# Kernel tuning notes

Hardware: AMD Instinct MI355X
Metric: run time of the kernel (lower is better)

The kernel has to match this reference:

```python
import jax, jax.numpy as jnp
import numpy as np

HD = 64        # hidden_dim
H = 4          # heads
N = 50000      # nodes
E = 400000     # edges (before self loops)
NEG_ATT = 0.2  # GATConv attention LeakyReLU slope (PyG default)
NEG_ACT = 0.01 # nn.LeakyReLU() default slope
EPS = 1e-5     # BatchNorm eps


def _bn(x, gamma, beta):
    # training-mode BatchNorm1d over node dimension (biased variance)
    mu = x.mean(0)
    var = x.var(0)
    return gamma * (x - mu) * jax.lax.rsqrt(var + EPS) + beta


def _gatconv(h_in, src, dst, W, a_src, a_dst, bias, heads, outc, concat):
    n = h_in.shape[0]
    h = (h_in @ W.T).reshape(n, heads, outc)              # [N,H,C]
    al_s = jnp.einsum('nhc,hc->nh', h, a_src)             # [N,H]
    al_d = jnp.einsum('nhc,hc->nh', h, a_dst)
    e = jax.nn.leaky_relu(al_s[src] + al_d[dst], NEG_ATT) # [E',H]
    # softmax over incoming edges of each destination node
    m = jax.lax.stop_gradient(jax.ops.segment_max(e, dst, num_segments=n))
    ex = jnp.exp(e - m[dst])
    den = jax.ops.segment_sum(ex, dst, num_segments=n)
    alpha = ex / den[dst]                                  # [E',H]
    out = jax.ops.segment_sum(h[src] * alpha[..., None], dst, num_segments=n)
    out = out.reshape(n, heads * outc) if concat else out.mean(axis=1)
    return out + bias


def setup_inputs() -> dict:
    ks = jax.random.split(jax.random.key(0), 20)
    s = 0.1
    d = {
        'x': jax.random.normal(ks[0], (N, 2 * HD), jnp.float32),
        'edge_index': jax.random.randint(ks[1], (2, E), 0, N, jnp.int64),
        'W1': jax.random.normal(ks[2], (H * HD, 2 * HD), jnp.float32) * s,
        'a1s': jax.random.normal(ks[3], (H, HD), jnp.float32) * s,
        'a1d': jax.random.normal(ks[4], (H, HD), jnp.float32) * s,
        'b1': jnp.zeros((H * HD,), jnp.float32),
        'W2': jax.random.normal(ks[5], (H * HD, H * HD), jnp.float32) * s,
        'a2s': jax.random.normal(ks[6], (H, HD), jnp.float32) * s,
        'a2d': jax.random.normal(ks[7], (H, HD), jnp.float32) * s,
        'b2': jnp.zeros((H * HD,), jnp.float32),
        'W3': jax.random.normal(ks[8], (1 * HD, H * HD), jnp.float32) * s,
        'a3s': jax.random.normal(ks[9], (1, HD), jnp.float32) * s,
        'a3d': jax.random.normal(ks[10], (1, HD), jnp.float32) * s,
        'b3': jnp.zeros((HD,), jnp.float32),
        'gamma': jnp.ones((H * HD,), jnp.float32),
        'beta': jnp.zeros((H * HD,), jnp.float32),
    }
    return d


def reference(x, edge_index, W1, a1s, a1d, b1, W2, a2s, a2d, b2,
              W3, a3s, a3d, b3, gamma, beta):
    n = x.shape[0]
    loop = jnp.arange(n, dtype=edge_index.dtype)
    src = jnp.concatenate([edge_index[0], loop])  # add_self_loops=True
    dst = jnp.concatenate([edge_index[1], loop])

    h = _gatconv(x, src, dst, W1, a1s, a1d, b1, H, HD, True)
    h = jax.nn.leaky_relu(_bn(h, gamma, beta), NEG_ACT)

    # single middle residual block (num_layers=3); dropout is identity (eval)
    res = h
    h = _gatconv(h, src, dst, W2, a2s, a2d, b2, H, HD, True)
    h = jax.nn.leaky_relu(_bn(h, gamma, beta), NEG_ACT)
    h = h + res

    out = _gatconv(h, src, dst, W3, a3s, a3d, b3, 1, HD, False)
    return out
```

## Files before the change

### kernel.cpp

```cpp
#include <hip/hip_runtime.h>
#include <hip/hip_bf16.h>

#define NEG_ATT 0.2f
#define NEG_ACT 0.01f

typedef __attribute__((ext_vector_type(8))) short short8;
typedef __attribute__((ext_vector_type(4))) float f32x4;

__device__ __forceinline__ unsigned short f2bf(float f) {
    unsigned int u = __float_as_uint(f);
    unsigned int r = (u + 0x7fff + ((u >> 16) & 1)) >> 16;
    return (unsigned short)r;
}
__device__ __forceinline__ float b2f(unsigned short h) {
    return __uint_as_float((unsigned int)h << 16);
}


#define SCAN_CHUNK 1024
__global__ void scan1(const int* __restrict__ deg, int* __restrict__ offs,
                      int* blocksum, int Nn) {
    __shared__ int sh[256];
    int b = blockIdx.x, t = threadIdx.x;
    int base = b * SCAN_CHUNK + t * 4;
    int v[4];
    int s = 0;
    for (int j = 0; j < 4; j++) {
        int idx = base + j;
        v[j] = (idx < Nn) ? deg[idx] + 1 : 0;
        s += v[j];
    }
    sh[t] = s;
    __syncthreads();
    for (int off = 1; off < 256; off <<= 1) {
        int x = (t >= off) ? sh[t - off] : 0;
        __syncthreads();
        sh[t] += x;
        __syncthreads();
    }
    int excl = sh[t] - s;
    if (t == 255) blocksum[b] = sh[255];
    int run = excl;
    for (int j = 0; j < 4; j++) {
        int idx = base + j;
        if (idx < Nn) offs[idx] = run;
        run += v[j];
    }
}

__global__ void scan23(int* __restrict__ offs, const int* __restrict__ bsum,
                       int* __restrict__ cursor, int Nn, int G) {
    int i = blockIdx.x * 256 + threadIdx.x;
    if (i > Nn) return;
    int g = i >> 10;
    int basev = 0;
    for (int k = 0; k < g; k++) basev += bsum[k];
    if (i == Nn) {
        int tot = basev;
        for (int k = g; k < G; k++) tot += bsum[k];
        offs[Nn] = tot;
        return;
    }
    int v = offs[i] + basev;
    offs[i] = v;
    cursor[i] = v;
}

__global__ void fill_csr(const int* __restrict__ ei, int* cursor, int* csr, int E, int Nn) {
    int t = blockIdx.x * 256 + threadIdx.x;
    if (t < E) {
        int s = ei[t];
        int d = ei[E + t];
        int p = atomicAdd(&cursor[d], 1);
        csr[p] = s;
    } else if (t < E + Nn) {
        int nn = t - E;
        int p = atomicAdd(&cursor[nn], 1);
        csr[p] = nn;
    }
}


__global__ __launch_bounds__(256) void prep_all(
    int* __restrict__ deg, const int* __restrict__ ei, int E,
    const float* __restrict__ x, unsigned short* __restrict__ xb, int nx, int nxpad,
    const float* __restrict__ w1, unsigned short* __restrict__ o1, int n1,
    const float* __restrict__ w2, unsigned short* __restrict__ o2, int n2,
    const float* __restrict__ w3, unsigned short* __restrict__ o3, int n3) {
    int id = blockIdx.x * 256 + threadIdx.x;
    int nconv = (nxpad + n1 + n2 + n3) / 8;
    if (id >= nconv) {
        int e = id - nconv;
        if (e < E) atomicAdd(&deg[ei[E + e]], 1);
        return;
    }
    int i = id * 8;
    const float* in;
    unsigned short* out;
    if (i < nxpad) {
        if (i >= nx) {
            *(ushort4*)&xb[i] = make_ushort4(0, 0, 0, 0);
            *(ushort4*)&xb[i + 4] = make_ushort4(0, 0, 0, 0);
            return;
        }
        in = x + i; out = xb + i;
    } else {
        int j = i - nxpad;
        if (j < n1) { in = w1 + j; out = o1 + j; }
        else if (j < n1 + n2) { in = w2 + (j - n1); out = o2 + (j - n1); }
        else { in = w3 + (j - n1 - n2); out = o3 + (j - n1 - n2); }
    }
    float4 a = *(const float4*)in;
    float4 b = *(const float4*)(in + 4);
    *(ushort4*)out = make_ushort4(f2bf(a.x), f2bf(a.y), f2bf(a.z), f2bf(a.w));
    *(ushort4*)(out + 4) = make_ushort4(f2bf(b.x), f2bf(b.y), f2bf(b.z), f2bf(b.w));
}

template <bool RES>
__device__ __forceinline__ unsigned bnpack2(unsigned short ya, unsigned short yb_,
                                            float sca, float scb, float sha, float shb,
                                            unsigned short ra, unsigned short rb_) {
    float v0 = sca * b2f(ya) + sha; v0 = v0 > 0.f ? v0 : NEG_ACT * v0;
    float v1 = scb * b2f(yb_) + shb; v1 = v1 > 0.f ? v1 : NEG_ACT * v1;
    if (RES) { v0 += b2f(ra); v1 += b2f(rb_); }
    return ((unsigned)f2bf(v1) << 16) | f2bf(v0);
}


template <int K, int CO, int HEADS, bool FUSE, bool FRES, bool FWOUT>
__global__ __launch_bounds__(256) void gemm_mfma(
    const unsigned short* __restrict__ Xb, const unsigned short* __restrict__ Wb,
    unsigned short* __restrict__ Hb, const float* __restrict__ a_s,
    const float* __restrict__ a_d, float* __restrict__ als, float* __restrict__ ald,
    const unsigned short* __restrict__ Yb_in, unsigned short* __restrict__ RWbuf,
    const float* __restrict__ scale, const float* __restrict__ shift, int Nn) {
    constexpr int BM = 128, BK = 64, LD = 72, SLD = 68;
    __shared__ __align__(16) char smem[4 * 32 * SLD * 4];
    unsigned short* As = (unsigned short*)smem;
    unsigned short* Bs = As + BM * LD;
    int tid = threadIdx.x;
    int wave = tid >> 6, lane = tid & 63;
    int quad = lane >> 4, l16 = lane & 15;
    int mt, hd;
    if (HEADS == 4) {
        int gm = gridDim.x >> 2;
        int gm8 = gm & ~7;
        int nfull = gm8 * 4;
        int id = blockIdx.x;
        if (id < nfull) {
            int r = id & 31;
            mt = (id >> 5) * 8 + (r & 7);
            hd = r >> 3;
        } else {
            int t2 = id - nfull;
            mt = gm8 + (t2 >> 2);
            hd = t2 & 3;
        }
    } else {
        mt = blockIdx.x;
        hd = 0;
    }
    int m0 = mt * BM, n0 = hd * 64;
    int arow = tid >> 3;
    int achk = (tid & 7) * 8;
    f32x4 acc[2][4] = {};
    for (int k0 = 0; k0 < K; k0 += BK) {
        __syncthreads();
        if (FUSE) {
            int cb = k0 + achk;
            float4 sc0 = *(const float4*)&scale[cb];
            float4 sc1 = *(const float4*)&scale[cb + 4];
            float4 sh0 = *(const float4*)&shift[cb];
            float4 sh1 = *(const float4*)&shift[cb + 4];
#pragma unroll
            for (int p = 0; p < 4; p++) {
                int r = arow + p * 32;
                int m = m0 + r;
                uint4 o = make_uint4(0, 0, 0, 0);
                if (m < Nn) {
                    ushort4 ua = *(const ushort4*)&Yb_in[(size_t)m * 256 + cb];
                    ushort4 ub = *(const ushort4*)&Yb_in[(size_t)m * 256 + cb + 4];
                    ushort4 ra = make_ushort4(0, 0, 0, 0), rb = ra;
                    if (FRES) {
                        ra = *(const ushort4*)&RWbuf[(size_t)m * 256 + cb];
                        rb = *(const ushort4*)&RWbuf[(size_t)m * 256 + cb + 4];
                    }
                    o.x = bnpack2<FRES>(ua.x, ua.y, sc0.x, sc0.y, sh0.x, sh0.y, ra.x, ra.y);
                    o.y = bnpack2<FRES>(ua.z, ua.w, sc0.z, sc0.w, sh0.z, sh0.w, ra.z, ra.w);
                    o.z = bnpack2<FRES>(ub.x, ub.y, sc1.x, sc1.y, sh1.x, sh1.y, rb.x, rb.y);
                    o.w = bnpack2<FRES>(ub.z, ub.w, sc1.z, sc1.w, sh1.z, sh1.w, rb.z, rb.w);
                    if (FWOUT && hd == 0)
                        *(uint4*)&RWbuf[(size_t)m * 256 + cb] = o;
                }
                *(uint4*)&As[r * LD + achk] = o;
            }
        } else {
#pragma unroll
            for (int p = 0; p < 4; p++) {
                int r = arow + p * 32;
                *(int4*)&As[r * LD + achk] = *(const int4*)&Xb[(size_t)(m0 + r) * K + k0 + achk];
            }
        }
#pragma unroll
        for (int p = 0; p < 2; p++) {
            int r = arow + p * 32;
            *(int4*)&Bs[r * LD + achk] = *(const int4*)&Wb[(size_t)(n0 + r) * K + k0 + achk];
        }
        __syncthreads();
#pragma unroll
        for (int ks = 0; ks < 2; ks++) {
            short8 af[2], bfr[4];
#pragma unroll
            for (int i = 0; i < 2; i++)
                af[i] = *(const short8*)&As[(wave * 32 + i * 16 + l16) * LD + ks * 32 + quad * 8];
#pragma unroll
            for (int j = 0; j < 4; j++)
                bfr[j] = *(const short8*)&Bs[(j * 16 + l16) * LD + ks * 32 + quad * 8];
#pragma unroll
            for (int i = 0; i < 2; i++)
#pragma unroll
                for (int j = 0; j < 4; j++)
                    acc[i][j] = __builtin_amdgcn_mfma_f32_16x16x32_bf16(af[i], bfr[j], acc[i][j], 0, 0, 0);
        }
    }
    __syncthreads();

    float asv[4], adv[4];
#pragma unroll
    for (int j = 0; j < 4; j++) {
        asv[j] = a_s[hd * 64 + j * 16 + l16];
        adv[j] = a_d[hd * 64 + j * 16 + l16];
    }
#pragma unroll
    for (int i = 0; i < 2; i++)
#pragma unroll
        for (int r = 0; r < 4; r++) {
            float ps = acc[i][0][r] * asv[0] + acc[i][1][r] * asv[1] +
                       acc[i][2][r] * asv[2] + acc[i][3][r] * asv[3];
            float pd = acc[i][0][r] * adv[0] + acc[i][1][r] * adv[1] +
                       acc[i][2][r] * adv[2] + acc[i][3][r] * adv[3];
#pragma unroll
            for (int mm = 1; mm < 16; mm <<= 1) {
                ps += __shfl_xor(ps, mm);
                pd += __shfl_xor(pd, mm);
            }
            if (l16 == 0) {
                int m = m0 + wave * 32 + i * 16 + quad * 4 + r;
                als[m * HEADS + hd] = ps;
                ald[m * HEADS + hd] = pd;
            }
        }

    float* stg = (float*)smem + wave * 32 * SLD;
#pragma unroll
    for (int i = 0; i < 2; i++)
#pragma unroll
        for (int j = 0; j < 4; j++)
#pragma unroll
            for (int r = 0; r < 4; r++)
                stg[(i * 16 + quad * 4 + r) * SLD + j * 16 + l16] = acc[i][j][r];
    int g = lane >> 3, c8 = (lane & 7) * 8;
#pragma unroll
    for (int p = 0; p < 4; p++) {
        int row = p * 8 + g;
        float4 v0 = *(const float4*)&stg[row * SLD + c8];
        float4 v1 = *(const float4*)&stg[row * SLD + c8 + 4];
        uint4 o;
        o.x = ((unsigned)f2bf(v0.y) << 16) | f2bf(v0.x);
        o.y = ((unsigned)f2bf(v0.w) << 16) | f2bf(v0.z);
        o.z = ((unsigned)f2bf(v1.y) << 16) | f2bf(v1.x);
        o.w = ((unsigned)f2bf(v1.w) << 16) | f2bf(v1.z);
        *(uint4*)&Hb[(size_t)(m0 + wave * 32 + row) * CO + n0 + c8] = o;
    }
}


#define EDGE4(sA, sB, sC, sD)                                                        \
    {                                                                                \
        float a0 = als[(sA)*4 + hd], a1 = als[(sB)*4 + hd];                          \
        float a2 = als[(sC)*4 + hd], a3 = als[(sD)*4 + hd];                          \
        ushort4 h0 = *(const ushort4*)&Hb[(size_t)(sA)*256 + c4];                    \
        ushort4 h1 = *(const ushort4*)&Hb[(size_t)(sB)*256 + c4];                    \
        ushort4 h2 = *(const ushort4*)&Hb[(size_t)(sC)*256 + c4];                    \
        ushort4 h3 = *(const ushort4*)&Hb[(size_t)(sD)*256 + c4];                    \
        float e0 = a0 + aldn; e0 = e0 > 0.f ? e0 : NEG_ATT * e0;                     \
        float e1 = a1 + aldn; e1 = e1 > 0.f ? e1 : NEG_ATT * e1;                     \
        float e2 = a2 + aldn; e2 = e2 > 0.f ? e2 : NEG_ATT * e2;                     \
        float e3 = a3 + aldn; e3 = e3 > 0.f ? e3 : NEG_ATT * e3;                     \
        float w0 = __expf(e0), w1 = __expf(e1), w2 = __expf(e2), w3 = __expf(e3);    \
        den += (w0 + w1) + (w2 + w3);                                                \
        acc.x += w0 * b2f(h0.x) + w1 * b2f(h1.x) + w2 * b2f(h2.x) + w3 * b2f(h3.x);  \
        acc.y += w0 * b2f(h0.y) + w1 * b2f(h1.y) + w2 * b2f(h2.y) + w3 * b2f(h3.y);  \
        acc.z += w0 * b2f(h0.z) + w1 * b2f(h1.z) + w2 * b2f(h2.z) + w3 * b2f(h3.z);  \
        acc.w += w0 * b2f(h0.w) + w1 * b2f(h1.w) + w2 * b2f(h2.w) + w3 * b2f(h3.w);  \
    }

__global__ __launch_bounds__(256) void aggregate_h4(
    const unsigned short* __restrict__ Hb, const float* __restrict__ als,
    const float* __restrict__ ald, const int* __restrict__ offs,
    const int* __restrict__ csr, unsigned short* __restrict__ Yb, int Nn) {
    int wave = threadIdx.x >> 6;
    int lane = threadIdx.x & 63;
    int n = blockIdx.x * 4 + wave;
    if (n >= Nn) return;
    int hd = lane >> 4;
    int c4 = lane * 4;
    float aldn = ald[n * 4 + hd];
    int beg = offs[n], end = offs[n + 1];
    float4 acc = make_float4(0.f, 0.f, 0.f, 0.f);
    float den = 0.f;
    for (int b = beg; b < end; b += 64) {
        int cnt = min(64, end - b);
        int idx = 0;
        if (lane < cnt) idx = csr[b + lane];
        int j = 0;
        for (; j + 8 <= cnt; j += 8) {
            int s0 = __shfl(idx, j), s1 = __shfl(idx, j + 1);
            int s2 = __shfl(idx, j + 2), s3 = __shfl(idx, j + 3);
            int s4 = __shfl(idx, j + 4), s5 = __shfl(idx, j + 5);
            int s6 = __shfl(idx, j + 6), s7 = __shfl(idx, j + 7);
            EDGE4(s0, s1, s2, s3);
            EDGE4(s4, s5, s6, s7);
        }
        for (; j + 4 <= cnt; j += 4) {
            int s0 = __shfl(idx, j), s1 = __shfl(idx, j + 1);
            int s2 = __shfl(idx, j + 2), s3 = __shfl(idx, j + 3);
            EDGE4(s0, s1, s2, s3);
        }
        for (; j < cnt; j++) {
            int s = __shfl(idx, j);
            float e = als[s * 4 + hd] + aldn;
            e = e > 0.f ? e : NEG_ATT * e;
            float w = __expf(e);
            den += w;
            ushort4 hv = *(const ushort4*)&Hb[(size_t)s * 256 + c4];
            acc.x += w * b2f(hv.x); acc.y += w * b2f(hv.y);
            acc.z += w * b2f(hv.z); acc.w += w * b2f(hv.w);
        }
    }
    float inv = 1.f / den;
    *(ushort4*)&Yb[(size_t)n * 256 + c4] = make_ushort4(
        f2bf(acc.x * inv), f2bf(acc.y * inv), f2bf(acc.z * inv), f2bf(acc.w * inv));
}

__global__ __launch_bounds__(256) void aggregate_h1(
    const unsigned short* __restrict__ Hb, const float* __restrict__ als,
    const float* __restrict__ ald, const int* __restrict__ offs,
    const int* __restrict__ csr, const float* __restrict__ bias,
    float* __restrict__ Yout, int Nn) {
    int wave = threadIdx.x >> 6;
    int lane = threadIdx.x & 63;
    int sub = lane >> 4, lane16 = lane & 15;
    int n = blockIdx.x * 16 + wave * 4 + sub;
    if (n >= Nn) return;
    int c4 = lane16 * 4;
    float aldn = ald[n];
    int beg = offs[n], end = offs[n + 1];
    float4 acc = make_float4(0.f, 0.f, 0.f, 0.f);
    float den = 0.f;
    for (int b = beg; b < end; b += 16) {
        int cnt = min(16, end - b);
        int idx = 0;
        if (lane16 < cnt) idx = csr[b + lane16];
        int j = 0;
        for (; j + 4 <= cnt; j += 4) {
            int s0 = __shfl(idx, (sub << 4) + j);
            int s1 = __shfl(idx, (sub << 4) + j + 1);
            int s2 = __shfl(idx, (sub << 4) + j + 2);
            int s3 = __shfl(idx, (sub << 4) + j + 3);
            float a0 = als[s0], a1 = als[s1], a2 = als[s2], a3 = als[s3];
            ushort4 h0 = *(const ushort4*)&Hb[(size_t)s0 * 64 + c4];
            ushort4 h1 = *(const ushort4*)&Hb[(size_t)s1 * 64 + c4];
            ushort4 h2 = *(const ushort4*)&Hb[(size_t)s2 * 64 + c4];
            ushort4 h3 = *(const ushort4*)&Hb[(size_t)s3 * 64 + c4];
            float e0 = a0 + aldn; e0 = e0 > 0.f ? e0 : NEG_ATT * e0;
            float e1 = a1 + aldn; e1 = e1 > 0.f ? e1 : NEG_ATT * e1;
            float e2 = a2 + aldn; e2 = e2 > 0.f ? e2 : NEG_ATT * e2;
            float e3 = a3 + aldn; e3 = e3 > 0.f ? e3 : NEG_ATT * e3;
            float w0 = __expf(e0), w1 = __expf(e1), w2 = __expf(e2), w3 = __expf(e3);
            den += (w0 + w1) + (w2 + w3);
            acc.x += w0 * b2f(h0.x) + w1 * b2f(h1.x) + w2 * b2f(h2.x) + w3 * b2f(h3.x);
            acc.y += w0 * b2f(h0.y) + w1 * b2f(h1.y) + w2 * b2f(h2.y) + w3 * b2f(h3.y);
            acc.z += w0 * b2f(h0.z) + w1 * b2f(h1.z) + w2 * b2f(h2.z) + w3 * b2f(h3.z);
            acc.w += w0 * b2f(h0.w) + w1 * b2f(h1.w) + w2 * b2f(h2.w) + w3 * b2f(h3.w);
        }
        for (; j < cnt; j++) {
            int s = __shfl(idx, (sub << 4) + j);
            float e = als[s] + aldn;
            e = e > 0.f ? e : NEG_ATT * e;
            float w = __expf(e);
            den += w;
            ushort4 hv = *(const ushort4*)&Hb[(size_t)s * 64 + c4];
            acc.x += w * b2f(hv.x); acc.y += w * b2f(hv.y);
            acc.z += w * b2f(hv.z); acc.w += w * b2f(hv.w);
        }
    }
    float inv = 1.f / den;
    float4 bv = *(const float4*)&bias[c4];
    float4 o = make_float4(acc.x * inv + bv.x, acc.y * inv + bv.y,
                           acc.z * inv + bv.z, acc.w * inv + bv.w);
    *(float4*)&Yout[(size_t)n * 64 + c4] = o;
}


__global__ __launch_bounds__(256) void bn_stats(const unsigned short* __restrict__ Yb,
                                                float* __restrict__ partial, int Nn) {
    __shared__ float red[4 * 512];
    int t = threadIdx.x;
    int g = blockIdx.x;
    int rows_per = (Nn + gridDim.x - 1) / gridDim.x;
    int r0 = g * rows_per;
    int r1 = min(r0 + rows_per, Nn);
    int sub = t >> 6;
    int c4 = (t & 63) * 4;
    float4 s = make_float4(0.f, 0.f, 0.f, 0.f);
    float4 q = make_float4(0.f, 0.f, 0.f, 0.f);
    for (int r = r0 + sub; r < r1; r += 4) {
        ushort4 u = *(const ushort4*)&Yb[(size_t)r * 256 + c4];
        float vx = b2f(u.x), vy = b2f(u.y), vz = b2f(u.z), vw = b2f(u.w);
        s.x += vx; s.y += vy; s.z += vz; s.w += vw;
        q.x += vx * vx; q.y += vy * vy; q.z += vz * vz; q.w += vw * vw;
    }
    float* rs = &red[sub * 512];
    rs[c4 + 0] = s.x; rs[c4 + 1] = s.y; rs[c4 + 2] = s.z; rs[c4 + 3] = s.w;
    rs[256 + c4 + 0] = q.x; rs[256 + c4 + 1] = q.y;
    rs[256 + c4 + 2] = q.z; rs[256 + c4 + 3] = q.w;
    __syncthreads();
    float v0 = red[t] + red[512 + t] + red[1024 + t] + red[1536 + t];
    float v1 = red[256 + t] + red[768 + t] + red[1280 + t] + red[1792 + t];
    partial[(size_t)g * 512 + t] = v0;
    partial[(size_t)g * 512 + 256 + t] = v1;
}

__global__ __launch_bounds__(256) void bn_reduce_final(
    const float* __restrict__ partial, int NP, const float* __restrict__ gamma,
    const float* __restrict__ beta, float* scale, float* shift, int Nn) {
    __shared__ float sh[8];
    int ch = blockIdx.x;
    int t = threadIdx.x;
    int wave = t >> 6, lane = t & 63;
    float s = 0.f, q = 0.f;
    for (int i = t; i < NP; i += 256) {
        s += partial[(size_t)i * 512 + ch];
        q += partial[(size_t)i * 512 + 256 + ch];
    }
    for (int off = 32; off; off >>= 1) {
        s += __shfl_down(s, off);
        q += __shfl_down(q, off);
    }
    if (lane == 0) { sh[wave] = s; sh[4 + wave] = q; }
    __syncthreads();
    if (t == 0) {
        s = sh[0] + sh[1] + sh[2] + sh[3];
        q = sh[4] + sh[5] + sh[6] + sh[7];
        float inv_n = 1.f / (float)Nn;
        float mu = s * inv_n;
        float var = q * inv_n - mu * mu;
        float sc = gamma[ch] * rsqrtf(var + 1e-5f);
        scale[ch] = sc;
        shift[ch] = beta[ch] - mu * sc;
    }
}


extern "C" void kernel_launch(void* const* d_in, const int* in_sizes, int n_in,
                              void* d_out, int out_size, void* d_ws, size_t ws_size,
                              hipStream_t stream) {
    const float* x    = (const float*)d_in[0];
    const int*   ei   = (const int*)d_in[1];
    const float* W1   = (const float*)d_in[2];
    const float* a1s  = (const float*)d_in[3];
    const float* a1d  = (const float*)d_in[4];
    const float* W2   = (const float*)d_in[6];
    const float* a2s  = (const float*)d_in[7];
    const float* a2d  = (const float*)d_in[8];
    const float* W3   = (const float*)d_in[10];
    const float* a3s  = (const float*)d_in[11];
    const float* a3d  = (const float*)d_in[12];
    const float* b3   = (const float*)d_in[13];
    const float* gamma = (const float*)d_in[14];
    const float* beta  = (const float*)d_in[15];
    float* out = (float*)d_out;

    const int Nn = in_sizes[0] / 128;
    const int E  = in_sizes[1] / 2;
    const int Ep = E + Nn;
    const int Mpad = (Nn + 127) & ~127;

    size_t off = 0;
    char* base = (char*)d_ws;
    auto alloc = [&](size_t bytes) -> void* {
        void* p = base + off;
        off = (off + bytes + 255) & ~(size_t)255;
        return p;
    };
    unsigned short* Hb   = (unsigned short*)alloc((size_t)Mpad * 256 * 2);
    unsigned short* Yb   = (unsigned short*)alloc((size_t)Nn * 256 * 2);
    unsigned short* xb1  = (unsigned short*)alloc((size_t)Mpad * 128 * 2);
    unsigned short* xbig = (unsigned short*)alloc((size_t)Mpad * 256 * 2);
    unsigned short* wb1  = (unsigned short*)alloc((size_t)256 * 128 * 2);
    unsigned short* wb2  = (unsigned short*)alloc((size_t)256 * 256 * 2);
    unsigned short* wb3  = (unsigned short*)alloc((size_t)64 * 256 * 2);
    float* als    = (float*)alloc((size_t)Mpad * 4 * 4);
    float* ald    = (float*)alloc((size_t)Mpad * 4 * 4);
    int*   deg    = (int*)alloc((size_t)Nn * 4);
    int*   offs   = (int*)alloc((size_t)(Nn + 1) * 4);
    int*   cursor = (int*)alloc((size_t)Nn * 4);
    int*   bsum   = (int*)alloc(64 * 4);
    int*   csr    = (int*)alloc((size_t)Ep * 4);
    const int NP = 1024;
    float* partial = (float*)alloc((size_t)NP * 512 * 4);
    float* scale  = (float*)alloc(256 * 4);
    float* shift  = (float*)alloc(256 * 4);
    (void)ws_size;

    const int G = (Nn + SCAN_CHUNK - 1) / SCAN_CHUNK;

    hipMemsetAsync(deg, 0, (size_t)Nn * 4, stream);
    {
        int nxpad = Mpad * 128;
        int wtot = 256 * 128 + 256 * 256 + 64 * 256;
        int nconv = (nxpad + wtot) / 8;
        prep_all<<<(nconv + E + 255) / 256, 256, 0, stream>>>(
            deg, ei, E, x, xb1, Nn * 128, nxpad,
            W1, wb1, 256 * 128, W2, wb2, 256 * 256, W3, wb3, 64 * 256);
    }

    scan1<<<G, 256, 0, stream>>>(deg, offs, bsum, Nn);
    scan23<<<(Nn + 1 + 255) / 256, 256, 0, stream>>>(offs, bsum, cursor, Nn, G);
    fill_csr<<<(Ep + 255) / 256, 256, 0, stream>>>(ei, cursor, csr, E, Nn);

    const int gm = Mpad / 128;
    const int nagg4 = (Nn + 3) / 4;
    const int nagg1 = (Nn + 15) / 16;

    gemm_mfma<128, 256, 4, false, false, false><<<gm * 4, 256, 0, stream>>>(
        xb1, wb1, Hb, a1s, a1d, als, ald, nullptr, nullptr, nullptr, nullptr, 0);
    aggregate_h4<<<nagg4, 256, 0, stream>>>(Hb, als, ald, offs, csr, Yb, Nn);
    bn_stats<<<NP, 256, 0, stream>>>(Yb, partial, Nn);
    bn_reduce_final<<<256, 256, 0, stream>>>(partial, NP, gamma, beta, scale, shift, Nn);

    gemm_mfma<256, 256, 4, true, false, true><<<gm * 4, 256, 0, stream>>>(
        nullptr, wb2, Hb, a2s, a2d, als, ald, Yb, xbig, scale, shift, Nn);
    aggregate_h4<<<nagg4, 256, 0, stream>>>(Hb, als, ald, offs, csr, Yb, Nn);
    bn_stats<<<NP, 256, 0, stream>>>(Yb, partial, Nn);
    bn_reduce_final<<<256, 256, 0, stream>>>(partial, NP, gamma, beta, scale, shift, Nn);

    gemm_mfma<256, 64, 1, true, true, false><<<gm, 256, 0, stream>>>(
        nullptr, wb3, Hb, a3s, a3d, als, ald, Yb, xbig, scale, shift, Nn);
    aggregate_h1<<<nagg1, 256, 0, stream>>>(Hb, als, ald, offs, csr, b3, out, Nn);
}
```

Baseline: 329.1 us.

## Fuse BatchNorm statistics into aggregation and use hardware bf16 pack conversion

```diff
diff --git a/kernel.cpp b/kernel.cpp
--- a/kernel.cpp
+++ b/kernel.cpp
@@ -7,13 +7,13 @@
 typedef __attribute__((ext_vector_type(8))) short short8;
 typedef __attribute__((ext_vector_type(4))) float f32x4;
 
-__device__ __forceinline__ unsigned short f2bf(float f) {
-    unsigned int u = __float_as_uint(f);
-    unsigned int r = (u + 0x7fff + ((u >> 16) & 1)) >> 16;
-    return (unsigned short)r;
-}
 __device__ __forceinline__ float b2f(unsigned short h) {
     return __uint_as_float((unsigned int)h << 16);
+}
+__device__ __forceinline__ unsigned cvt_pk_bf16(float lo, float hi) {
+    unsigned r;
+    asm("v_cvt_pk_bf16_f32 %0, %1, %2" : "=v"(r) : "v"(lo), "v"(hi));
+    return r;
 }
 
 
@@ -112,8 +112,12 @@
     }
     float4 a = *(const float4*)in;
     float4 b = *(const float4*)(in + 4);
-    *(ushort4*)out = make_ushort4(f2bf(a.x), f2bf(a.y), f2bf(a.z), f2bf(a.w));
-    *(ushort4*)(out + 4) = make_ushort4(f2bf(b.x), f2bf(b.y), f2bf(b.z), f2bf(b.w));
+    uint4 o;
+    o.x = cvt_pk_bf16(a.x, a.y);
+    o.y = cvt_pk_bf16(a.z, a.w);
+    o.z = cvt_pk_bf16(b.x, b.y);
+    o.w = cvt_pk_bf16(b.z, b.w);
+    *(uint4*)out = o;
 }
 
 template <bool RES>
@@ -123,7 +127,7 @@
     float v0 = sca * b2f(ya) + sha; v0 = v0 > 0.f ? v0 : NEG_ACT * v0;
     float v1 = scb * b2f(yb_) + shb; v1 = v1 > 0.f ? v1 : NEG_ACT * v1;
     if (RES) { v0 += b2f(ra); v1 += b2f(rb_); }
-    return ((unsigned)f2bf(v1) << 16) | f2bf(v0);
+    return cvt_pk_bf16(v0, v1);
 }
 
 
@@ -266,10 +270,10 @@
         float4 v0 = *(const float4*)&stg[row * SLD + c8];
         float4 v1 = *(const float4*)&stg[row * SLD + c8 + 4];
         uint4 o;
-        o.x = ((unsigned)f2bf(v0.y) << 16) | f2bf(v0.x);
-        o.y = ((unsigned)f2bf(v0.w) << 16) | f2bf(v0.z);
-        o.z = ((unsigned)f2bf(v1.y) << 16) | f2bf(v1.x);
-        o.w = ((unsigned)f2bf(v1.w) << 16) | f2bf(v1.z);
+        o.x = cvt_pk_bf16(v0.x, v0.y);
+        o.y = cvt_pk_bf16(v0.z, v0.w);
+        o.z = cvt_pk_bf16(v1.x, v1.y);
+        o.w = cvt_pk_bf16(v1.z, v1.w);
         *(uint4*)&Hb[(size_t)(m0 + wave * 32 + row) * CO + n0 + c8] = o;
     }
 }
@@ -298,49 +302,68 @@
 __global__ __launch_bounds__(256) void aggregate_h4(
     const unsigned short* __restrict__ Hb, const float* __restrict__ als,
     const float* __restrict__ ald, const int* __restrict__ offs,
-    const int* __restrict__ csr, unsigned short* __restrict__ Yb, int Nn) {
+    const int* __restrict__ csr, unsigned short* __restrict__ Yb,
+    float* __restrict__ S, int Nn) {
+    __shared__ float red[4 * 512];
     int wave = threadIdx.x >> 6;
     int lane = threadIdx.x & 63;
-    int n = blockIdx.x * 4 + wave;
-    if (n >= Nn) return;
     int hd = lane >> 4;
     int c4 = lane * 4;
-    float aldn = ald[n * 4 + hd];
-    int beg = offs[n], end = offs[n + 1];
-    float4 acc = make_float4(0.f, 0.f, 0.f, 0.f);
-    float den = 0.f;
-    for (int b = beg; b < end; b += 64) {
-        int cnt = min(64, end - b);
-        int idx = 0;
-        if (lane < cnt) idx = csr[b + lane];
-        int j = 0;
-        for (; j + 8 <= cnt; j += 8) {
-            int s0 = __shfl(idx, j), s1 = __shfl(idx, j + 1);
-            int s2 = __shfl(idx, j + 2), s3 = __shfl(idx, j + 3);
-            int s4 = __shfl(idx, j + 4), s5 = __shfl(idx, j + 5);
-            int s6 = __shfl(idx, j + 6), s7 = __shfl(idx, j + 7);
-            EDGE4(s0, s1, s2, s3);
-            EDGE4(s4, s5, s6, s7);
-        }
-        for (; j + 4 <= cnt; j += 4) {
-            int s0 = __shfl(idx, j), s1 = __shfl(idx, j + 1);
-            int s2 = __shfl(idx, j + 2), s3 = __shfl(idx, j + 3);
-            EDGE4(s0, s1, s2, s3);
-        }
-        for (; j < cnt; j++) {
-            int s = __shfl(idx, j);
-            float e = als[s * 4 + hd] + aldn;
-            e = e > 0.f ? e : NEG_ATT * e;
-            float w = __expf(e);
-            den += w;
-            ushort4 hv = *(const ushort4*)&Hb[(size_t)s * 256 + c4];
-            acc.x += w * b2f(hv.x); acc.y += w * b2f(hv.y);
-            acc.z += w * b2f(hv.z); acc.w += w * b2f(hv.w);
-        }
-    }
-    float inv = 1.f / den;
-    *(ushort4*)&Yb[(size_t)n * 256 + c4] = make_ushort4(
-        f2bf(acc.x * inv), f2bf(acc.y * inv), f2bf(acc.z * inv), f2bf(acc.w * inv));
+    float4 bs = make_float4(0.f, 0.f, 0.f, 0.f);
+    float4 bq = make_float4(0.f, 0.f, 0.f, 0.f);
+    for (int n = blockIdx.x * 4 + wave; n < Nn; n += gridDim.x * 4) {
+        float aldn = ald[n * 4 + hd];
+        int beg = offs[n], end = offs[n + 1];
+        float4 acc = make_float4(0.f, 0.f, 0.f, 0.f);
+        float den = 0.f;
+        for (int b = beg; b < end; b += 64) {
+            int cnt = min(64, end - b);
+            int idx = 0;
+            if (lane < cnt) idx = csr[b + lane];
+            int j = 0;
+            for (; j + 8 <= cnt; j += 8) {
+                int s0 = __shfl(idx, j), s1 = __shfl(idx, j + 1);
+                int s2 = __shfl(idx, j + 2), s3 = __shfl(idx, j + 3);
+                int s4 = __shfl(idx, j + 4), s5 = __shfl(idx, j + 5);
+                int s6 = __shfl(idx, j + 6), s7 = __shfl(idx, j + 7);
+                EDGE4(s0, s1, s2, s3);
+                EDGE4(s4, s5, s6, s7);
+            }
+            for (; j + 4 <= cnt; j += 4) {
+                int s0 = __shfl(idx, j), s1 = __shfl(idx, j + 1);
+                int s2 = __shfl(idx, j + 2), s3 = __shfl(idx, j + 3);
+                EDGE4(s0, s1, s2, s3);
+            }
+            for (; j < cnt; j++) {
+                int s = __shfl(idx, j);
+                float e = als[s * 4 + hd] + aldn;
+                e = e > 0.f ? e : NEG_ATT * e;
+                float w = __expf(e);
+                den += w;
+                ushort4 hv = *(const ushort4*)&Hb[(size_t)s * 256 + c4];
+                acc.x += w * b2f(hv.x); acc.y += w * b2f(hv.y);
+                acc.z += w * b2f(hv.z); acc.w += w * b2f(hv.w);
+            }
+        }
+        float inv = 1.f / den;
+        float yx = acc.x * inv, yy = acc.y * inv, yz = acc.z * inv, yw = acc.w * inv;
+        uint2 o;
+        o.x = cvt_pk_bf16(yx, yy);
+        o.y = cvt_pk_bf16(yz, yw);
+        *(uint2*)&Yb[(size_t)n * 256 + c4] = o;
+        bs.x += yx; bs.y += yy; bs.z += yz; bs.w += yw;
+        bq.x += yx * yx; bq.y += yy * yy; bq.z += yz * yz; bq.w += yw * yw;
+    }
+    float* rs = &red[wave * 512];
+    rs[c4 + 0] = bs.x; rs[c4 + 1] = bs.y; rs[c4 + 2] = bs.z; rs[c4 + 3] = bs.w;
+    rs[256 + c4 + 0] = bq.x; rs[256 + c4 + 1] = bq.y;
+    rs[256 + c4 + 2] = bq.z; rs[256 + c4 + 3] = bq.w;
+    __syncthreads();
+    int t = threadIdx.x;
+    float v0 = red[t] + red[512 + t] + red[1024 + t] + red[1536 + t];
+    float v1 = red[256 + t] + red[768 + t] + red[1280 + t] + red[1792 + t];
+    atomicAdd(&S[t], v0);
+    atomicAdd(&S[256 + t], v1);
 }
 
 __global__ __launch_bounds__(256) void aggregate_h1(
@@ -403,63 +426,16 @@
 }
 
 
-__global__ __launch_bounds__(256) void bn_stats(const unsigned short* __restrict__ Yb,
-                                                float* __restrict__ partial, int Nn) {
-    __shared__ float red[4 * 512];
-    int t = threadIdx.x;
-    int g = blockIdx.x;
-    int rows_per = (Nn + gridDim.x - 1) / gridDim.x;
-    int r0 = g * rows_per;
-    int r1 = min(r0 + rows_per, Nn);
-    int sub = t >> 6;
-    int c4 = (t & 63) * 4;
-    float4 s = make_float4(0.f, 0.f, 0.f, 0.f);
-    float4 q = make_float4(0.f, 0.f, 0.f, 0.f);
-    for (int r = r0 + sub; r < r1; r += 4) {
-        ushort4 u = *(const ushort4*)&Yb[(size_t)r * 256 + c4];
-        float vx = b2f(u.x), vy = b2f(u.y), vz = b2f(u.z), vw = b2f(u.w);
-        s.x += vx; s.y += vy; s.z += vz; s.w += vw;
-        q.x += vx * vx; q.y += vy * vy; q.z += vz * vz; q.w += vw * vw;
-    }
-    float* rs = &red[sub * 512];
-    rs[c4 + 0] = s.x; rs[c4 + 1] = s.y; rs[c4 + 2] = s.z; rs[c4 + 3] = s.w;
-    rs[256 + c4 + 0] = q.x; rs[256 + c4 + 1] = q.y;
-    rs[256 + c4 + 2] = q.z; rs[256 + c4 + 3] = q.w;
-    __syncthreads();
-    float v0 = red[t] + red[512 + t] + red[1024 + t] + red[1536 + t];
-    float v1 = red[256 + t] + red[768 + t] + red[1280 + t] + red[1792 + t];
-    partial[(size_t)g * 512 + t] = v0;
-    partial[(size_t)g * 512 + 256 + t] = v1;
-}
-
-__global__ __launch_bounds__(256) void bn_reduce_final(
-    const float* __restrict__ partial, int NP, const float* __restrict__ gamma,
-    const float* __restrict__ beta, float* scale, float* shift, int Nn) {
-    __shared__ float sh[8];
-    int ch = blockIdx.x;
-    int t = threadIdx.x;
-    int wave = t >> 6, lane = t & 63;
-    float s = 0.f, q = 0.f;
-    for (int i = t; i < NP; i += 256) {
-        s += partial[(size_t)i * 512 + ch];
-        q += partial[(size_t)i * 512 + 256 + ch];
-    }
-    for (int off = 32; off; off >>= 1) {
-        s += __shfl_down(s, off);
-        q += __shfl_down(q, off);
-    }
-    if (lane == 0) { sh[wave] = s; sh[4 + wave] = q; }
-    __syncthreads();
-    if (t == 0) {
-        s = sh[0] + sh[1] + sh[2] + sh[3];
-        q = sh[4] + sh[5] + sh[6] + sh[7];
-        float inv_n = 1.f / (float)Nn;
-        float mu = s * inv_n;
-        float var = q * inv_n - mu * mu;
-        float sc = gamma[ch] * rsqrtf(var + 1e-5f);
-        scale[ch] = sc;
-        shift[ch] = beta[ch] - mu * sc;
-    }
+__global__ __launch_bounds__(256) void bn_final(
+    const float* __restrict__ S, const float* __restrict__ gamma,
+    const float* __restrict__ beta, float* __restrict__ scale,
+    float* __restrict__ shift, float inv_n) {
+    int ch = threadIdx.x;
+    float mu = S[ch] * inv_n;
+    float var = S[256 + ch] * inv_n - mu * mu;
+    float sc = gamma[ch] * rsqrtf(var + 1e-5f);
+    scale[ch] = sc;
+    shift[ch] = beta[ch] - mu * sc;
 }
 
 
@@ -503,20 +479,24 @@
     unsigned short* wb3  = (unsigned short*)alloc((size_t)64 * 256 * 2);
     float* als    = (float*)alloc((size_t)Mpad * 4 * 4);
     float* ald    = (float*)alloc((size_t)Mpad * 4 * 4);
+    size_t zoff0 = off;
     int*   deg    = (int*)alloc((size_t)Nn * 4);
+    float* sums   = (float*)alloc(1024 * 4);
+    size_t zbytes = off - zoff0;
     int*   offs   = (int*)alloc((size_t)(Nn + 1) * 4);
     int*   cursor = (int*)alloc((size_t)Nn * 4);
     int*   bsum   = (int*)alloc(64 * 4);
     int*   csr    = (int*)alloc((size_t)Ep * 4);
-    const int NP = 1024;
-    float* partial = (float*)alloc((size_t)NP * 512 * 4);
     float* scale  = (float*)alloc(256 * 4);
     float* shift  = (float*)alloc(256 * 4);
     (void)ws_size;
 
+    float* sums0 = sums;
+    float* sums1 = sums + 512;
+
     const int G = (Nn + SCAN_CHUNK - 1) / SCAN_CHUNK;
 
-    hipMemsetAsync(deg, 0, (size_t)Nn * 4, stream);
+    hipMemsetAsync(deg, 0, zbytes, stream);
     {
         int nxpad = Mpad * 128;
         int wtot = 256 * 128 + 256 * 256 + 64 * 256;
@@ -531,20 +511,19 @@
     fill_csr<<<(Ep + 255) / 256, 256, 0, stream>>>(ei, cursor, csr, E, Nn);
 
     const int gm = Mpad / 128;
-    const int nagg4 = (Nn + 3) / 4;
+    const int NAGG = 2048;
     const int nagg1 = (Nn + 15) / 16;
+    const float inv_n = 1.f / (float)Nn;
 
     gemm_mfma<128, 256, 4, false, false, false><<<gm * 4, 256, 0, stream>>>(
         xb1, wb1, Hb, a1s, a1d, als, ald, nullptr, nullptr, nullptr, nullptr, 0);
-    aggregate_h4<<<nagg4, 256, 0, stream>>>(Hb, als, ald, offs, csr, Yb, Nn);
-    bn_stats<<<NP, 256, 0, stream>>>(Yb, partial, Nn);
-    bn_reduce_final<<<256, 256, 0, stream>>>(partial, NP, gamma, beta, scale, shift, Nn);
+    aggregate_h4<<<NAGG, 256, 0, stream>>>(Hb, als, ald, offs, csr, Yb, sums0, Nn);
+    bn_final<<<1, 256, 0, stream>>>(sums0, gamma, beta, scale, shift, inv_n);
 
     gemm_mfma<256, 256, 4, true, false, true><<<gm * 4, 256, 0, stream>>>(
         nullptr, wb2, Hb, a2s, a2d, als, ald, Yb, xbig, scale, shift, Nn);
-    aggregate_h4<<<nagg4, 256, 0, stream>>>(Hb, als, ald, offs, csr, Yb, Nn);
-    bn_stats<<<NP, 256, 0, stream>>>(Yb, partial, Nn);
-    bn_reduce_final<<<256, 256, 0, stream>>>(partial, NP, gamma, beta, scale, shift, Nn);
+    aggregate_h4<<<NAGG, 256, 0, stream>>>(Hb, als, ald, offs, csr, Yb, sums1, Nn);
+    bn_final<<<1, 256, 0, stream>>>(sums1, gamma, beta, scale, shift, inv_n);
 
     gemm_mfma<256, 64, 1, true, true, false><<<gm, 256, 0, stream>>>(
         nullptr, wb3, Hb, a3s, a3d, als, ald, Yb, xbig, scale, shift, Nn);
```

New measurement: 383.2 us. 1.16x slower.
